# Performance work log

Hardware: AMD Instinct MI355X
Metric: run time of the kernel (lower is better)

The kernel has to match this reference:

```python
import jax, jax.numpy as jnp
import numpy as np

N_NODES = 50000
N_EDGES = 800000
IN_DIM = 128
HID = 32
HEADS = 4
OUT_DIM = 64
NEG_SLOPE = 0.2


def _glorot(key, shape):
    fan = shape[0] + shape[-1] if len(shape) > 1 else shape[-1]
    lim = jnp.sqrt(6.0 / fan)
    return jax.random.uniform(key, shape, jnp.float32, -lim, lim)


def setup_inputs() -> dict:
    key = jax.random.key(0)
    ks = jax.random.split(key, 10)
    x = jax.random.normal(ks[0], (N_NODES, IN_DIM), jnp.float32)
    edge_index = jax.random.randint(ks[1], (2, N_EDGES), 0, N_NODES, jnp.int32)
    # layer 1: in=IN_DIM, heads=HEADS, out=HID, concat
    W1 = _glorot(ks[2], (IN_DIM, HEADS * HID))
    a_src1 = _glorot(ks[3], (HEADS, HID))
    a_dst1 = _glorot(ks[4], (HEADS, HID))
    b1 = jnp.zeros((HEADS * HID,), jnp.float32)
    # layer 2: in=HEADS*HID, heads=1, out=OUT_DIM, mean
    W2 = _glorot(ks[5], (HEADS * HID, OUT_DIM))
    a_src2 = _glorot(ks[6], (1, OUT_DIM))
    a_dst2 = _glorot(ks[7], (1, OUT_DIM))
    b2 = jnp.zeros((OUT_DIM,), jnp.float32)
    return {"x": x, "edge_index": edge_index, "W1": W1, "a_src1": a_src1,
            "a_dst1": a_dst1, "b1": b1, "W2": W2, "a_src2": a_src2,
            "a_dst2": a_dst2, "b2": b2}


def gat_conv(x, src, dst, W, a_src, a_dst, bias, heads, out_ch, concat, num_nodes):
    # x: [N, in]; src/dst: [E] (self-loops already included)
    h = (x @ W).reshape(num_nodes, heads, out_ch)          # [N, H, F]
    alpha_s = jnp.einsum('nhf,hf->nh', h, a_src)           # [N, H]
    alpha_d = jnp.einsum('nhf,hf->nh', h, a_dst)
    e = alpha_s[src] + alpha_d[dst]                        # [E, H]
    e = jnp.where(e >= 0, e, NEG_SLOPE * e)                # leaky relu
    # segment softmax over destination neighborhoods
    e_max = jax.ops.segment_max(e, dst, num_segments=num_nodes)
    ex = jnp.exp(e - e_max[dst])
    denom = jax.ops.segment_sum(ex, dst, num_segments=num_nodes)
    alpha = ex / (denom[dst] + 1e-16)                      # [E, H]
    msg = h[src] * alpha[:, :, None]                       # [E, H, F]
    out = jax.ops.segment_sum(msg, dst, num_segments=num_nodes)  # [N, H, F]
    if concat:
        out = out.reshape(num_nodes, heads * out_ch)
    else:
        out = out.mean(axis=1)
    return out + bias


def reference(x, edge_index, W1, a_src1, a_dst1, b1, W2, a_src2, a_dst2, b2):
    n = x.shape[0]
    # PyG GATConv default add_self_loops=True
    loop = jnp.arange(n, dtype=edge_index.dtype)
    src = jnp.concatenate([edge_index[0], loop])
    dst = jnp.concatenate([edge_index[1], loop])
    h = gat_conv(x, src, dst, W1, a_src1, a_dst1, b1, HEADS, HID, True, n)
    h = jax.nn.relu(h)
    out = gat_conv(h, src, dst, W2, a_src2, a_dst2, b2, 1, OUT_DIM, False, n)
    return out
```

## Files before the change

### kernel.cpp

```cpp
#include <hip/hip_runtime.h>
#include <hip/hip_fp16.h>
#include <math.h>


#define NEG_SLOPE 0.2f
#define CAP 64
#define DEGS 32

typedef _Float16 f16x8 __attribute__((ext_vector_type(8)));
typedef float    f32x4 __attribute__((ext_vector_type(4)));

__device__ __forceinline__ float lrelu_exp(float e) {
    e = (e >= 0.f) ? e : NEG_SLOPE * e;
    return __expf(e);
}

__global__ __launch_bounds__(256, 4) void build_kernel(
    const float* __restrict__ x, const float* __restrict__ W1,
    const float* __restrict__ a_src1, const float* __restrict__ a_dst1,
    __half* __restrict__ h1h, float* __restrict__ as1, float* __restrict__ ad1,
    const int* __restrict__ src, const int* __restrict__ dst,
    int* __restrict__ deg, unsigned short* __restrict__ col,
    int N, int E, int Gs) {
    __shared__ __half hs[64 * 136];
    const int tid = threadIdx.x;

    if (blockIdx.x < Gs) {
        const int base = blockIdx.x * 2048 + tid * 8;
        int s[8], d[8];
        if (base + 8 <= E) {
            int4 a0 = *(const int4*)&src[base];
            int4 a1 = *(const int4*)&src[base + 4];
            int4 c0 = *(const int4*)&dst[base];
            int4 c1 = *(const int4*)&dst[base + 4];
            s[0]=a0.x; s[1]=a0.y; s[2]=a0.z; s[3]=a0.w;
            s[4]=a1.x; s[5]=a1.y; s[6]=a1.z; s[7]=a1.w;
            d[0]=c0.x; d[1]=c0.y; d[2]=c0.z; d[3]=c0.w;
            d[4]=c1.x; d[5]=c1.y; d[6]=c1.z; d[7]=c1.w;
        } else {
#pragma unroll
            for (int u = 0; u < 8; ++u) {
                int i = base + u;
                if (i < E) { s[u] = src[i]; d[u] = dst[i]; }
                else       { s[u] = -1;     d[u] = -1; }
            }
        }
        int p[8];
#pragma unroll
        for (int u = 0; u < 8; ++u)
            if (d[u] >= 0) p[u] = atomicAdd(&deg[(size_t)d[u] * DEGS], 1);
#pragma unroll
        for (int u = 0; u < 8; ++u)
            if (d[u] >= 0 && p[u] < CAP)
                col[d[u] * CAP + p[u]] = (unsigned short)s[u];
        return;
    }

    const int w    = tid >> 6;
    const int lane = tid & 63;
    const int r16  = lane & 15;
    const int g4   = lane >> 4;
    const int nb   = (blockIdx.x - Gs) * 64;

    f16x8 bf[2][4];
#pragma unroll
    for (int ct = 0; ct < 2; ++ct) {
        const int c = w * 32 + ct * 16 + r16;
#pragma unroll
        for (int ks = 0; ks < 4; ++ks) {
            const float* wp = W1 + (size_t)(ks * 32 + g4 * 8) * 128 + c;
            f16x8 b;
#pragma unroll
            for (int j = 0; j < 8; ++j)
                b[j] = (_Float16)wp[(size_t)j * 128];
            bf[ct][ks] = b;
        }
    }

    f32x4 acc[4][2];
#pragma unroll
    for (int rt = 0; rt < 4; ++rt)
#pragma unroll
        for (int ct = 0; ct < 2; ++ct)
            acc[rt][ct] = (f32x4){0.f, 0.f, 0.f, 0.f};

#pragma unroll
    for (int rt = 0; rt < 4; ++rt) {
        int gr = nb + rt * 16 + r16;
        if (gr >= N) gr = N - 1;
        const float* xp = x + (size_t)gr * 128 + g4 * 8;
        f16x8 af[4];
#pragma unroll
        for (int ks = 0; ks < 4; ++ks) {
            float4 u0 = *(const float4*)(xp + ks * 32);
            float4 u1 = *(const float4*)(xp + ks * 32 + 4);
            f16x8 a;
            a[0] = (_Float16)u0.x; a[1] = (_Float16)u0.y;
            a[2] = (_Float16)u0.z; a[3] = (_Float16)u0.w;
            a[4] = (_Float16)u1.x; a[5] = (_Float16)u1.y;
            a[6] = (_Float16)u1.z; a[7] = (_Float16)u1.w;
            af[ks] = a;
        }
#pragma unroll
        for (int ct = 0; ct < 2; ++ct)
#pragma unroll
            for (int ks = 0; ks < 4; ++ks)
                acc[rt][ct] = __builtin_amdgcn_mfma_f32_16x16x32_f16(
                    af[ks], bf[ct][ks], acc[rt][ct], 0, 0, 0);
    }

#pragma unroll
    for (int rt = 0; rt < 4; ++rt)
#pragma unroll
        for (int ct = 0; ct < 2; ++ct) {
            const int c = w * 32 + ct * 16 + r16;
#pragma unroll
            for (int i = 0; i < 4; ++i) {
                const int r = rt * 16 + g4 * 4 + i;
                hs[r * 136 + c] = __float2half(acc[rt][ct][i]);
            }
        }
    __syncthreads();

#pragma unroll
    for (int p = 0; p < 4; ++p) {
        const int idx = tid + p * 256;
        const int row = idx >> 4;
        const int c8  = (idx & 15) << 3;
        const int gn  = nb + row;
        if (gn < N)
            *(uint4*)&h1h[(size_t)gn * 128 + c8] =
                *(const uint4*)&hs[row * 136 + c8];
    }

    {
        const int row  = tid >> 2;
        const int head = tid & 3;
        const int gn   = nb + row;
        if (gn < N) {
            const __half* hp = &hs[row * 136 + head * 32];
            float s = 0.f, dv = 0.f;
#pragma unroll
            for (int f4 = 0; f4 < 8; ++f4) {
                float4 av = *(const float4*)&a_src1[head * 32 + f4 * 4];
                float4 bv = *(const float4*)&a_dst1[head * 32 + f4 * 4];
                float2 h01 = __half22float2(*(const __half2*)&hp[f4 * 4]);
                float2 h23 = __half22float2(*(const __half2*)&hp[f4 * 4 + 2]);
                s  += h01.x * av.x + h01.y * av.y + h23.x * av.z + h23.y * av.w;
                dv += h01.x * bv.x + h01.y * bv.y + h23.x * bv.z + h23.y * bv.w;
            }
            as1[(size_t)gn * 4 + head] = s;
            ad1[(size_t)gn * 4 + head] = dv;
        }
    }
}

__global__ __launch_bounds__(256) void agg1mm_kernel(
    const __half2* __restrict__ h1h2, const float* __restrict__ as1,
    const float* __restrict__ ad1, const float* __restrict__ b1,
    const float* __restrict__ W2, const float* __restrict__ a_src2,
    const float* __restrict__ a_dst2, const int* __restrict__ deg,
    const unsigned short* __restrict__ col,
    __half* __restrict__ h2h, float* __restrict__ as2, float* __restrict__ ad2,
    int N) {
    __shared__ float wls[4][4][68];
    __shared__ int   cls[4][64];
    __shared__ float hrs[4][128];
    __shared__ float part[16][64];
    const int tid = threadIdx.x;
    const int w = tid >> 6;
    const int lane = tid & 63;
    const int d = blockIdx.x * 4 + w;

    if (d < N) {
        const int hsel = lane >> 4;
        const float4 ad4 = *(const float4*)&ad1[4 * d];
        const float4 asd = *(const float4*)&as1[4 * d];
        const float adh = (hsel == 0) ? ad4.x : (hsel == 1) ? ad4.y
                        : (hsel == 2) ? ad4.z : ad4.w;
        const float ash = (hsel == 0) ? asd.x : (hsel == 1) ? asd.y
                        : (hsel == 2) ? asd.z : asd.w;
        const int dg = min(deg[(size_t)d * DEGS], CAP);
        const int dgp = (dg + 15) & ~15;
        const int beg = d * CAP;

        if (lane < dgp) {
            if (lane < dg) {
                int s = (int)col[beg + lane];
                cls[w][lane] = s;
                float4 a4 = *(const float4*)&as1[4 * s];
                wls[w][0][lane] = lrelu_exp(a4.x + ad4.x);
                wls[w][1][lane] = lrelu_exp(a4.y + ad4.y);
                wls[w][2][lane] = lrelu_exp(a4.z + ad4.z);
                wls[w][3][lane] = lrelu_exp(a4.w + ad4.w);
            } else {
                cls[w][lane] = 0;
                wls[w][0][lane] = 0.f;
                wls[w][1][lane] = 0.f;
                wls[w][2][lane] = 0.f;
                wls[w][3][lane] = 0.f;
            }
        }

        float wself = lrelu_exp(ash + adh);
        float2 vself = __half22float2(h1h2[((unsigned)d << 6) | (unsigned)lane]);
        float den = wself, accx = wself * vself.x, accy = wself * vself.y;

        for (int jj = 0; jj < dgp; jj += 16) {
            int4 c0 = *(const int4*)&cls[w][jj];
            int4 c1 = *(const int4*)&cls[w][jj + 4];
            int4 c2 = *(const int4*)&cls[w][jj + 8];
            int4 c3 = *(const int4*)&cls[w][jj + 12];
            int ss[16] = {c0.x, c0.y, c0.z, c0.w, c1.x, c1.y, c1.z, c1.w,
                          c2.x, c2.y, c2.z, c2.w, c3.x, c3.y, c3.z, c3.w};
            __half2 v[16];
#pragma unroll
            for (int u = 0; u < 16; ++u)
                v[u] = h1h2[(((unsigned)ss[u]) << 6) | (unsigned)lane];
            float4 w0 = *(const float4*)&wls[w][hsel][jj];
            float4 w1 = *(const float4*)&wls[w][hsel][jj + 4];
            float4 w2 = *(const float4*)&wls[w][hsel][jj + 8];
            float4 w3 = *(const float4*)&wls[w][hsel][jj + 12];
            float wt[16] = {w0.x, w0.y, w0.z, w0.w, w1.x, w1.y, w1.z, w1.w,
                            w2.x, w2.y, w2.z, w2.w, w3.x, w3.y, w3.z, w3.w};
#pragma unroll
            for (int u = 0; u < 16; ++u) {
                float2 vf = __half22float2(v[u]);
                den += wt[u];
                accx += wt[u] * vf.x;
                accy += wt[u] * vf.y;
            }
        }
        const float inv = 1.f / (den + 1e-16f);
        float2 bv = *(const float2*)&b1[lane * 2];
        float2 o;
        o.x = fmaxf(accx * inv + bv.x, 0.f);
        o.y = fmaxf(accy * inv + bv.y, 0.f);
        *(float2*)&hrs[w][lane * 2] = o;
    } else {
        hrs[w][lane * 2] = 0.f;
        hrs[w][lane * 2 + 1] = 0.f;
    }
    __syncthreads();

    float p0 = 0.f, p1 = 0.f, p2 = 0.f, p3 = 0.f;
#pragma unroll
    for (int kk = 0; kk < 32; kk += 4) {
        const int k = w * 32 + kk;
        float4 h0 = *(const float4*)&hrs[0][k];
        float4 h1 = *(const float4*)&hrs[1][k];
        float4 h2 = *(const float4*)&hrs[2][k];
        float4 h3 = *(const float4*)&hrs[3][k];
        float wv0 = W2[(k + 0) * 64 + lane];
        float wv1 = W2[(k + 1) * 64 + lane];
        float wv2 = W2[(k + 2) * 64 + lane];
        float wv3 = W2[(k + 3) * 64 + lane];
        p0 += h0.x * wv0 + h0.y * wv1 + h0.z * wv2 + h0.w * wv3;
        p1 += h1.x * wv0 + h1.y * wv1 + h1.z * wv2 + h1.w * wv3;
        p2 += h2.x * wv0 + h2.y * wv1 + h2.z * wv2 + h2.w * wv3;
        p3 += h3.x * wv0 + h3.y * wv1 + h3.z * wv2 + h3.w * wv3;
    }
    part[w * 4 + 0][lane] = p0;
    part[w * 4 + 1][lane] = p1;
    part[w * 4 + 2][lane] = p2;
    part[w * 4 + 3][lane] = p3;
    __syncthreads();

    if (d < N) {
        float h2f = part[0 * 4 + w][lane] + part[1 * 4 + w][lane] +
                    part[2 * 4 + w][lane] + part[3 * 4 + w][lane];
        h2h[((unsigned)d << 6) | (unsigned)lane] = __float2half(h2f);
        float s = h2f * a_src2[lane];
        float dv = h2f * a_dst2[lane];
        s += __shfl_down(s, 32); dv += __shfl_down(dv, 32);
        s += __shfl_down(s, 16); dv += __shfl_down(dv, 16);
        s += __shfl_down(s, 8);  dv += __shfl_down(dv, 8);
        s += __shfl_down(s, 4);  dv += __shfl_down(dv, 4);
        s += __shfl_down(s, 2);  dv += __shfl_down(dv, 2);
        s += __shfl_down(s, 1);  dv += __shfl_down(dv, 1);
        if (lane == 0) { as2[d] = s; ad2[d] = dv; }
    }
}

__global__ __launch_bounds__(256) void agg2_kernel(
    const __half* __restrict__ h2h, const float* __restrict__ as2,
    const float* __restrict__ ad2, const float* __restrict__ b2,
    const int* __restrict__ deg, const unsigned short* __restrict__ col,
    float* __restrict__ out, int N) {
    __shared__ int   cls[4][64];
    __shared__ float wl[4][64];
    const int lane = threadIdx.x & 63;
    const int w = threadIdx.x >> 6;
    const int d = blockIdx.x * 4 + w;
    if (d >= N) return;
    const int dg = min(deg[(size_t)d * DEGS], CAP);
    const int dgp = (dg + 15) & ~15;
    const int beg = d * CAP;
    const float adv = ad2[d];

    float wself = lrelu_exp(as2[d] + adv);
    float den = wself;
    float acc = wself * __half2float(h2h[((unsigned)d << 6) | (unsigned)lane]);

    if (lane < dgp) {
        if (lane < dg) {
            int s = (int)col[beg + lane];
            cls[w][lane] = s;
            wl[w][lane] = lrelu_exp(as2[s] + adv);
        } else {
            cls[w][lane] = 0;
            wl[w][lane] = 0.f;
        }
    }

    for (int jj = 0; jj < dgp; jj += 16) {
        int4 c0 = *(const int4*)&cls[w][jj];
        int4 c1 = *(const int4*)&cls[w][jj + 4];
        int4 c2 = *(const int4*)&cls[w][jj + 8];
        int4 c3 = *(const int4*)&cls[w][jj + 12];
        int ss[16] = {c0.x, c0.y, c0.z, c0.w, c1.x, c1.y, c1.z, c1.w,
                      c2.x, c2.y, c2.z, c2.w, c3.x, c3.y, c3.z, c3.w};
        __half v[16];
#pragma unroll
        for (int u = 0; u < 16; ++u)
            v[u] = h2h[(((unsigned)ss[u]) << 6) | (unsigned)lane];
        float4 w0 = *(const float4*)&wl[w][jj];
        float4 w1 = *(const float4*)&wl[w][jj + 4];
        float4 w2 = *(const float4*)&wl[w][jj + 8];
        float4 w3 = *(const float4*)&wl[w][jj + 12];
        float wt[16] = {w0.x, w0.y, w0.z, w0.w, w1.x, w1.y, w1.z, w1.w,
                        w2.x, w2.y, w2.z, w2.w, w3.x, w3.y, w3.z, w3.w};
#pragma unroll
        for (int u = 0; u < 16; ++u) {
            den += wt[u];
            acc += wt[u] * __half2float(v[u]);
        }
    }
    out[(size_t)d * 64 + lane] = acc / (den + 1e-16f) + b2[lane];
}

extern "C" void kernel_launch(void* const* d_in, const int* in_sizes, int n_in,
                              void* d_out, int out_size, void* d_ws, size_t ws_size,
                              hipStream_t stream) {
    const float* x      = (const float*)d_in[0];
    const int*   eidx   = (const int*)d_in[1];
    const float* W1     = (const float*)d_in[2];
    const float* a_src1 = (const float*)d_in[3];
    const float* a_dst1 = (const float*)d_in[4];
    const float* b1     = (const float*)d_in[5];
    const float* W2     = (const float*)d_in[6];
    const float* a_src2 = (const float*)d_in[7];
    const float* a_dst2 = (const float*)d_in[8];
    const float* b2     = (const float*)d_in[9];
    float* out = (float*)d_out;

    const int N = in_sizes[0] / 128;
    const int E = in_sizes[1] / 2;

    const int* src = eidx;
    const int* dst = eidx + E;

    float* ws_f = (float*)d_ws;
    float* as1 = ws_f;
    float* ad1 = as1 + (size_t)N * 4;
    float* as2 = ad1 + (size_t)N * 4;
    float* ad2 = as2 + (size_t)N;
    __half* h1h = (__half*)(ad2 + (size_t)N);
    __half* h2h = h1h + (size_t)N * 128;
    int* deg = (int*)(h2h + (size_t)N * 64);
    unsigned short* col = (unsigned short*)(deg + (size_t)N * DEGS);

    const int Gs = (E + 2047) / 2048;
    const int Gg = (N + 63) / 64;

    hipMemsetAsync(deg, 0, (size_t)N * DEGS * sizeof(int), stream);

    build_kernel<<<Gs + Gg, 256, 0, stream>>>(x, W1, a_src1, a_dst1,
                                              h1h, as1, ad1,
                                              src, dst, deg, col, N, E, Gs);

    agg1mm_kernel<<<(N + 3) / 4, 256, 0, stream>>>(
        (const __half2*)h1h, as1, ad1, b1, W2, a_src2, a_dst2,
        deg, col, h2h, as2, ad2, N);

    agg2_kernel<<<(N + 3) / 4, 256, 0, stream>>>(h2h, as2, ad2, b2,
                                                 deg, col, out, N);
}
```

Measured before the change: 218.3 us.

## Pre-transpose W1 to fp16 in a prep kernel that also zeroes degree counters

A new prep kernel writes W1 as a transposed fp16 matrix and zeroes the degree array, replacing the hipMemsetAsync. The GEMM blocks can then load B fragments with one 16-byte vector load instead of eight strided fp32 loads each. The scatter blocks also handle 4 edges per thread instead of 8, which doubles the block count to add parallelism for the atomics. In exchange there is an extra kernel launch and a small extra workspace buffer.

```diff
diff --git a/kernel.cpp b/kernel.cpp
--- a/kernel.cpp
+++ b/kernel.cpp
@@ -15,8 +15,21 @@
     return __expf(e);
 }
 
+__global__ __launch_bounds__(256) void prep_kernel(
+    const float* __restrict__ W1, __half* __restrict__ w1t,
+    int* __restrict__ deg, int degWords) {
+    const int tid = blockIdx.x * 256 + threadIdx.x;
+    if (tid < 16384) {
+        const int k = tid >> 7, c = tid & 127;
+        w1t[c * 128 + k] = __float2half(W1[k * 128 + c]);
+    }
+    const int idx = tid * 4;
+    if (idx < degWords)
+        *(int4*)&deg[idx] = (int4){0, 0, 0, 0};
+}
+
 __global__ __launch_bounds__(256, 4) void build_kernel(
-    const float* __restrict__ x, const float* __restrict__ W1,
+    const float* __restrict__ x, const __half* __restrict__ w1t,
     const float* __restrict__ a_src1, const float* __restrict__ a_dst1,
     __half* __restrict__ h1h, float* __restrict__ as1, float* __restrict__ ad1,
     const int* __restrict__ src, const int* __restrict__ dst,
@@ -26,31 +39,27 @@
     const int tid = threadIdx.x;
 
     if (blockIdx.x < Gs) {
-        const int base = blockIdx.x * 2048 + tid * 8;
-        int s[8], d[8];
-        if (base + 8 <= E) {
-            int4 a0 = *(const int4*)&src[base];
-            int4 a1 = *(const int4*)&src[base + 4];
-            int4 c0 = *(const int4*)&dst[base];
-            int4 c1 = *(const int4*)&dst[base + 4];
-            s[0]=a0.x; s[1]=a0.y; s[2]=a0.z; s[3]=a0.w;
-            s[4]=a1.x; s[5]=a1.y; s[6]=a1.z; s[7]=a1.w;
-            d[0]=c0.x; d[1]=c0.y; d[2]=c0.z; d[3]=c0.w;
-            d[4]=c1.x; d[5]=c1.y; d[6]=c1.z; d[7]=c1.w;
+        const int base = blockIdx.x * 1024 + tid * 4;
+        int s[4], d[4];
+        if (base + 4 <= E) {
+            int4 a = *(const int4*)&src[base];
+            int4 c = *(const int4*)&dst[base];
+            s[0]=a.x; s[1]=a.y; s[2]=a.z; s[3]=a.w;
+            d[0]=c.x; d[1]=c.y; d[2]=c.z; d[3]=c.w;
         } else {
 #pragma unroll
-            for (int u = 0; u < 8; ++u) {
+            for (int u = 0; u < 4; ++u) {
                 int i = base + u;
                 if (i < E) { s[u] = src[i]; d[u] = dst[i]; }
                 else       { s[u] = -1;     d[u] = -1; }
             }
         }
-        int p[8];
-#pragma unroll
-        for (int u = 0; u < 8; ++u)
+        int p[4];
+#pragma unroll
+        for (int u = 0; u < 4; ++u)
             if (d[u] >= 0) p[u] = atomicAdd(&deg[(size_t)d[u] * DEGS], 1);
 #pragma unroll
-        for (int u = 0; u < 8; ++u)
+        for (int u = 0; u < 4; ++u)
             if (d[u] >= 0 && p[u] < CAP)
                 col[d[u] * CAP + p[u]] = (unsigned short)s[u];
         return;
@@ -67,14 +76,8 @@
     for (int ct = 0; ct < 2; ++ct) {
         const int c = w * 32 + ct * 16 + r16;
 #pragma unroll
-        for (int ks = 0; ks < 4; ++ks) {
-            const float* wp = W1 + (size_t)(ks * 32 + g4 * 8) * 128 + c;
-            f16x8 b;
-#pragma unroll
-            for (int j = 0; j < 8; ++j)
-                b[j] = (_Float16)wp[(size_t)j * 128];
-            bf[ct][ks] = b;
-        }
+        for (int ks = 0; ks < 4; ++ks)
+            bf[ct][ks] = *(const f16x8*)&w1t[c * 128 + ks * 32 + g4 * 8];
     }
 
     f32x4 acc[4][2];
@@ -369,13 +372,16 @@
     __half* h2h = h1h + (size_t)N * 128;
     int* deg = (int*)(h2h + (size_t)N * 64);
     unsigned short* col = (unsigned short*)(deg + (size_t)N * DEGS);
-
-    const int Gs = (E + 2047) / 2048;
+    __half* w1t = (__half*)(col + (size_t)N * CAP);
+
+    const int degWords = N * DEGS;
+    const int Gp = (degWords / 4 + 255) / 256;
+    const int Gs = (E + 1023) / 1024;
     const int Gg = (N + 63) / 64;
 
-    hipMemsetAsync(deg, 0, (size_t)N * DEGS * sizeof(int), stream);
-
-    build_kernel<<<Gs + Gg, 256, 0, stream>>>(x, W1, a_src1, a_dst1,
+    prep_kernel<<<Gp, 256, 0, stream>>>(W1, w1t, deg, degWords);
+
+    build_kernel<<<Gs + Gg, 256, 0, stream>>>(x, w1t, a_src1, a_dst1,
                                               h1h, as1, ad1,
                                               src, dst, deg, col, N, E, Gs);
 
```

New measurement: 219.6 us. No clear change (+0.6%).

## Shard degree counters across eight arrays and compact sentinel-filled adjacency slots

Applied to the files above, without the earlier changes.

Edge bucketing now uses eight sharded per-node counters, picked by block index, with a 12-slot region per shard and an overflow counter. This is meant to reduce contention on hot atomic addresses and replaces the padded 32-int stride counter layout. The aggregation kernels no longer read the degree. They scan 128 slots filled with a 0xFFFF sentinel and compact valid entries with ballot and popcount. A prep kernel replaces the memset: it pre-transposes W1 to fp16 and initialises the counters and slots. The cost is twice as many adjacency bytes to read and clear per node, and the 16-bit source id now collides with the sentinel for node id 65535.

```diff
diff --git a/kernel.cpp b/kernel.cpp
--- a/kernel.cpp
+++ b/kernel.cpp
@@ -4,8 +4,9 @@
 
 
 #define NEG_SLOPE 0.2f
-#define CAP 64
-#define DEGS 32
+#define SLOTS 128
+#define SHARD_CAP 12
+#define OV_BASE 96
 
 typedef _Float16 f16x8 __attribute__((ext_vector_type(8)));
 typedef float    f32x4 __attribute__((ext_vector_type(4)));
@@ -15,17 +16,36 @@
     return __expf(e);
 }
 
+__global__ __launch_bounds__(256) void prep_kernel(
+    const float* __restrict__ W1, __half* __restrict__ w1t,
+    int* __restrict__ deg8, unsigned short* __restrict__ col, int N) {
+    const int tid = blockIdx.x * 256 + threadIdx.x;
+    if (tid < 16384) {
+        const int k = tid >> 7, c = tid & 127;
+        w1t[c * 128 + k] = __float2half(W1[k * 128 + c]);
+    }
+    const int nz = (9 * N) >> 2;
+    if (tid < nz)
+        ((int4*)deg8)[tid] = (int4){0, 0, 0, 0};
+    const int nc = N * SLOTS / 8;
+    if (tid < nc)
+        ((uint4*)col)[tid] = (uint4){~0u, ~0u, ~0u, ~0u};
+}
+
 __global__ __launch_bounds__(256, 4) void build_kernel(
-    const float* __restrict__ x, const float* __restrict__ W1,
+    const float* __restrict__ x, const __half* __restrict__ w1t,
     const float* __restrict__ a_src1, const float* __restrict__ a_dst1,
     __half* __restrict__ h1h, float* __restrict__ as1, float* __restrict__ ad1,
     const int* __restrict__ src, const int* __restrict__ dst,
-    int* __restrict__ deg, unsigned short* __restrict__ col,
+    int* __restrict__ deg8, int* __restrict__ ov,
+    unsigned short* __restrict__ col,
     int N, int E, int Gs) {
     __shared__ __half hs[64 * 136];
     const int tid = threadIdx.x;
 
     if (blockIdx.x < Gs) {
+        const int shard = blockIdx.x & 7;
+        int* dcnt = deg8 + (size_t)shard * N;
         const int base = blockIdx.x * 2048 + tid * 8;
         int s[8], d[8];
         if (base + 8 <= E) {
@@ -48,11 +68,16 @@
         int p[8];
 #pragma unroll
         for (int u = 0; u < 8; ++u)
-            if (d[u] >= 0) p[u] = atomicAdd(&deg[(size_t)d[u] * DEGS], 1);
+            if (d[u] >= 0) p[u] = atomicAdd(&dcnt[d[u]], 1);
 #pragma unroll
         for (int u = 0; u < 8; ++u)
-            if (d[u] >= 0 && p[u] < CAP)
-                col[d[u] * CAP + p[u]] = (unsigned short)s[u];
+            if (d[u] >= 0) {
+                int slot = (p[u] < SHARD_CAP)
+                               ? shard * SHARD_CAP + p[u]
+                               : OV_BASE + atomicAdd(&ov[d[u]], 1);
+                if (slot < SLOTS)
+                    col[(size_t)d[u] * SLOTS + slot] = (unsigned short)s[u];
+            }
         return;
     }
 
@@ -67,14 +92,8 @@
     for (int ct = 0; ct < 2; ++ct) {
         const int c = w * 32 + ct * 16 + r16;
 #pragma unroll
-        for (int ks = 0; ks < 4; ++ks) {
-            const float* wp = W1 + (size_t)(ks * 32 + g4 * 8) * 128 + c;
-            f16x8 b;
-#pragma unroll
-            for (int j = 0; j < 8; ++j)
-                b[j] = (_Float16)wp[(size_t)j * 128];
-            bf[ct][ks] = b;
-        }
+        for (int ks = 0; ks < 4; ++ks)
+            bf[ct][ks] = *(const f16x8*)&w1t[c * 128 + ks * 32 + g4 * 8];
     }
 
     f32x4 acc[4][2];
@@ -159,12 +178,11 @@
     const __half2* __restrict__ h1h2, const float* __restrict__ as1,
     const float* __restrict__ ad1, const float* __restrict__ b1,
     const float* __restrict__ W2, const float* __restrict__ a_src2,
-    const float* __restrict__ a_dst2, const int* __restrict__ deg,
-    const unsigned short* __restrict__ col,
+    const float* __restrict__ a_dst2, const unsigned short* __restrict__ col,
     __half* __restrict__ h2h, float* __restrict__ as2, float* __restrict__ ad2,
     int N) {
-    __shared__ float wls[4][4][68];
-    __shared__ int   cls[4][64];
+    __shared__ float wls[4][4][132];
+    __shared__ int   cls[4][128];
     __shared__ float hrs[4][128];
     __shared__ float part[16][64];
     const int tid = threadIdx.x;
@@ -180,26 +198,46 @@
                         : (hsel == 2) ? ad4.z : ad4.w;
         const float ash = (hsel == 0) ? asd.x : (hsel == 1) ? asd.y
                         : (hsel == 2) ? asd.z : asd.w;
-        const int dg = min(deg[(size_t)d * DEGS], CAP);
+        const size_t beg = (size_t)d * SLOTS;
+
+        const unsigned short v0 = col[beg + lane];
+        const unsigned short v1 = col[beg + 64 + lane];
+        const bool ok0 = (v0 != 0xFFFFu);
+        const bool ok1 = (v1 != 0xFFFFu);
+        const unsigned long long bl0 = __ballot(ok0);
+        const unsigned long long bl1 = __ballot(ok1);
+        const unsigned long long ml = (1ull << lane) - 1ull;
+        const int n0 = __popcll(bl0);
+        const int dg = n0 + __popcll(bl1);
+        if (ok0) {
+            const int idx = __popcll(bl0 & ml);
+            const int s = (int)v0;
+            cls[w][idx] = s;
+            float4 a4 = *(const float4*)&as1[4 * s];
+            wls[w][0][idx] = lrelu_exp(a4.x + ad4.x);
+            wls[w][1][idx] = lrelu_exp(a4.y + ad4.y);
+            wls[w][2][idx] = lrelu_exp(a4.z + ad4.z);
+            wls[w][3][idx] = lrelu_exp(a4.w + ad4.w);
+        }
+        if (ok1) {
+            const int idx = n0 + __popcll(bl1 & ml);
+            const int s = (int)v1;
+            cls[w][idx] = s;
+            float4 a4 = *(const float4*)&as1[4 * s];
+            wls[w][0][idx] = lrelu_exp(a4.x + ad4.x);
+            wls[w][1][idx] = lrelu_exp(a4.y + ad4.y);
+            wls[w][2][idx] = lrelu_exp(a4.z + ad4.z);
+            wls[w][3][idx] = lrelu_exp(a4.w + ad4.w);
+        }
         const int dgp = (dg + 15) & ~15;
-        const int beg = d * CAP;
-
-        if (lane < dgp) {
-            if (lane < dg) {
-                int s = (int)col[beg + lane];
-                cls[w][lane] = s;
-                float4 a4 = *(const float4*)&as1[4 * s];
-                wls[w][0][lane] = lrelu_exp(a4.x + ad4.x);
-                wls[w][1][lane] = lrelu_exp(a4.y + ad4.y);
-                wls[w][2][lane] = lrelu_exp(a4.z + ad4.z);
-                wls[w][3][lane] = lrelu_exp(a4.w + ad4.w);
-            } else {
-                cls[w][lane] = 0;
-                wls[w][0][lane] = 0.f;
-                wls[w][1][lane] = 0.f;
-                wls[w][2][lane] = 0.f;
-                wls[w][3][lane] = 0.f;
-            }
+        const int padn = dgp - dg;
+        if (lane < padn) {
+            const int idx = dg + lane;
+            cls[w][idx] = 0;
+            wls[w][0][idx] = 0.f;
+            wls[w][1][idx] = 0.f;
+            wls[w][2][idx] = 0.f;
+            wls[w][3][idx] = 0.f;
         }
 
         float wself = lrelu_exp(ash + adh);
@@ -285,32 +323,45 @@
 __global__ __launch_bounds__(256) void agg2_kernel(
     const __half* __restrict__ h2h, const float* __restrict__ as2,
     const float* __restrict__ ad2, const float* __restrict__ b2,
-    const int* __restrict__ deg, const unsigned short* __restrict__ col,
+    const unsigned short* __restrict__ col,
     float* __restrict__ out, int N) {
-    __shared__ int   cls[4][64];
-    __shared__ float wl[4][64];
+    __shared__ int   cls[4][128];
+    __shared__ float wl[4][128];
     const int lane = threadIdx.x & 63;
     const int w = threadIdx.x >> 6;
     const int d = blockIdx.x * 4 + w;
     if (d >= N) return;
-    const int dg = min(deg[(size_t)d * DEGS], CAP);
-    const int dgp = (dg + 15) & ~15;
-    const int beg = d * CAP;
+    const size_t beg = (size_t)d * SLOTS;
     const float adv = ad2[d];
 
     float wself = lrelu_exp(as2[d] + adv);
     float den = wself;
     float acc = wself * __half2float(h2h[((unsigned)d << 6) | (unsigned)lane]);
 
-    if (lane < dgp) {
-        if (lane < dg) {
-            int s = (int)col[beg + lane];
-            cls[w][lane] = s;
-            wl[w][lane] = lrelu_exp(as2[s] + adv);
-        } else {
-            cls[w][lane] = 0;
-            wl[w][lane] = 0.f;
-        }
+    const unsigned short v0 = col[beg + lane];
+    const unsigned short v1 = col[beg + 64 + lane];
+    const bool ok0 = (v0 != 0xFFFFu);
+    const bool ok1 = (v1 != 0xFFFFu);
+    const unsigned long long bl0 = __ballot(ok0);
+    const unsigned long long bl1 = __ballot(ok1);
+    const unsigned long long ml = (1ull << lane) - 1ull;
+    const int n0 = __popcll(bl0);
+    const int dg = n0 + __popcll(bl1);
+    if (ok0) {
+        const int idx = __popcll(bl0 & ml);
+        cls[w][idx] = (int)v0;
+        wl[w][idx] = lrelu_exp(as2[(int)v0] + adv);
+    }
+    if (ok1) {
+        const int idx = n0 + __popcll(bl1 & ml);
+        cls[w][idx] = (int)v1;
+        wl[w][idx] = lrelu_exp(as2[(int)v1] + adv);
+    }
+    const int dgp = (dg + 15) & ~15;
+    const int padn = dgp - dg;
+    if (lane < padn) {
+        cls[w][dg + lane] = 0;
+        wl[w][dg + lane] = 0.f;
     }
 
     for (int jj = 0; jj < dgp; jj += 16) {
@@ -367,22 +418,25 @@
     float* ad2 = as2 + (size_t)N;
     __half* h1h = (__half*)(ad2 + (size_t)N);
     __half* h2h = h1h + (size_t)N * 128;
-    int* deg = (int*)(h2h + (size_t)N * 64);
-    unsigned short* col = (unsigned short*)(deg + (size_t)N * DEGS);
-
+    int* deg8 = (int*)(h2h + (size_t)N * 64);
+    int* ov   = deg8 + (size_t)8 * N;
+    unsigned short* col = (unsigned short*)(ov + N);
+    __half* w1t = (__half*)(col + (size_t)N * SLOTS);
+
+    const int Gp = (N * SLOTS / 8 + 255) / 256;
     const int Gs = (E + 2047) / 2048;
     const int Gg = (N + 63) / 64;
 
-    hipMemsetAsync(deg, 0, (size_t)N * DEGS * sizeof(int), stream);
-
-    build_kernel<<<Gs + Gg, 256, 0, stream>>>(x, W1, a_src1, a_dst1,
+    prep_kernel<<<Gp, 256, 0, stream>>>(W1, w1t, deg8, col, N);
+
+    build_kernel<<<Gs + Gg, 256, 0, stream>>>(x, w1t, a_src1, a_dst1,
                                               h1h, as1, ad1,
-                                              src, dst, deg, col, N, E, Gs);
+                                              src, dst, deg8, ov, col, N, E, Gs);
 
     agg1mm_kernel<<<(N + 3) / 4, 256, 0, stream>>>(
         (const __half2*)h1h, as1, ad1, b1, W2, a_src2, a_dst2,
-        deg, col, h2h, as2, ad2, N);
+        col, h2h, as2, ad2, N);
 
     agg2_kernel<<<(N + 3) / 4, 256, 0, stream>>>(h2h, as2, ad2, b2,
-                                                 deg, col, out, N);
-}
+                                                 col, out, N);
+}
```

Result: no change. 214.6 us (-1.7%).
